# Optimization experiments

Measured on AMD Instinct MI355X. Metric: run time of the kernel, lower is better.

## Reference

```python
import jax, jax.numpy as jnp
import numpy as np

B, T, C = 4, 2048, 1024
H, D = 16, 64  # n_head, head_dim; H*D == C
EPS = 1e-12


def _l2norm(x):
    # matches torch F.normalize(dim=-1): x / max(||x||_2, eps)
    n = jnp.sqrt(jnp.sum(x * x, axis=-1, keepdims=True))
    return x / jnp.maximum(n, EPS)


def setup_inputs() -> dict:
    key = jax.random.key(0)
    ks = jax.random.split(key, 8)
    s = 0.02
    return {
        "x": jax.random.normal(ks[0], (B, T, C), dtype=jnp.float32),
        "Wq": jax.random.normal(ks[1], (C, C), dtype=jnp.float32) * s,
        "Wk": jax.random.normal(ks[2], (C, C), dtype=jnp.float32) * s,
        "Wv": jax.random.normal(ks[3], (C, C), dtype=jnp.float32) * s,
        "Wbeta": jax.random.normal(ks[4], (H, C), dtype=jnp.float32) * s,
        "bbeta": jnp.zeros((H,), dtype=jnp.float32),
        "Wgate": jax.random.normal(ks[5], (C, C), dtype=jnp.float32) * s,
        "Wo": jax.random.normal(ks[6], (C, C), dtype=jnp.float32) * s,
    }


def _forward(x, Wq, Wk, Wv, Wbeta, bbeta, Wgate, Wo):
    q = (x @ Wq.T).reshape(B, T, H, D)
    k = (x @ Wk.T).reshape(B, T, H, D)
    v = (x @ Wv.T).reshape(B, T, H, D)
    beta = jax.nn.sigmoid(x @ Wbeta.T + bbeta)  # (B,T,H)
    gate = jax.nn.sigmoid(x @ Wgate.T)          # (B,T,C)

    q = _l2norm(q)
    k = _l2norm(k)

    # time-major for scan: (T,B,H,D) / (T,B,H)
    qT = jnp.transpose(q, (1, 0, 2, 3))
    kT = jnp.transpose(k, (1, 0, 2, 3))
    vT = jnp.transpose(v, (1, 0, 2, 3))
    bT = jnp.transpose(beta, (1, 0, 2))

    M0 = jnp.zeros((B, H, D, D), dtype=x.dtype)

    def step(M, inp):
        q_t, k_t, v_t, b_t = inp
        o_t = jnp.einsum('bhdc,bhc->bhd', M, q_t)       # read state with q (pre-update)
        Mk = jnp.einsum('bhdc,bhc->bhd', M, k_t)
        dv = v_t - Mk                                    # delta-rule error
        M = M + b_t[..., None, None] * jnp.einsum('bhd,bhc->bhdc', dv, k_t)
        return M, o_t

    _, oT = jax.lax.scan(step, M0, (qT, kT, vT, bT))     # oT: (T,B,H,D)
    o = jnp.transpose(oT, (1, 0, 2, 3)).reshape(B, T, C)
    return (gate * o) @ Wo.T


def reference(x, Wq, Wk, Wv, Wbeta, bbeta, Wgate, Wo):
    return _forward(x, Wq, Wk, Wv, Wbeta, bbeta, Wgate, Wo)
```

## Files before the change

kernel.cpp:

```cpp
#include <hip/hip_runtime.h>
#include <cstdint>
#include <cstddef>

#define Bz 4
#define Tz 2048
#define Cz 1024
#define Hz 16
#define Dz 64
#define NTOK (Bz*Tz)
#define CHL 32
#define NCH (Tz/CHL)

typedef __attribute__((ext_vector_type(8))) short  short8;
typedef __attribute__((ext_vector_type(4))) float  floatx4;

__device__ __forceinline__ unsigned short f2bf(float x) {
  union { float f; uint32_t u; } a; a.f = x;
  uint32_t r = a.u + 0x7fffu + ((a.u >> 16) & 1u);
  return (unsigned short)(r >> 16);
}
__device__ __forceinline__ float bf2f(unsigned short u) {
  union { uint32_t i; float f; } a; a.i = ((uint32_t)u) << 16; return a.f;
}
__device__ __forceinline__ float sigmoidf_(float z) {
  return 1.0f / (1.0f + __expf(-z));
}
__device__ __forceinline__ uint32_t cvtpk_bf16(float a, float b) {
  uint32_t d;
  asm volatile("v_cvt_pk_bf16_f32 %0, %1, %2" : "=v"(d) : "v"(a), "v"(b));
  return d;
}
__device__ __forceinline__ float lo16f(uint32_t u) {
  union { uint32_t i; float f; } a; a.i = u << 16; return a.f;
}
__device__ __forceinline__ float hi16f(uint32_t u) {
  union { uint32_t i; float f; } a; a.i = u & 0xffff0000u; return a.f;
}

__device__ __forceinline__ void gload_lds16(const void* gptr, void* lptr) {
  __builtin_amdgcn_global_load_lds(
      (const __attribute__((address_space(1))) void*)(uintptr_t)gptr,
      (__attribute__((address_space(3))) void*)(uint32_t)(uintptr_t)lptr,
      16, 0, 0);
}

template<int CTRL>
__device__ __forceinline__ float dpp_addf(float x) {
  int y = __builtin_amdgcn_update_dpp(0, __float_as_int(x), CTRL, 0xF, 0xF, true);
  return x + __int_as_float(y);
}
__device__ __forceinline__ float rowsum16(float x) {
  x = dpp_addf<0xB1>(x);
  x = dpp_addf<0x4E>(x);
  x = dpp_addf<0x124>(x);
  x = dpp_addf<0x128>(x);
  return x;
}

union FragU { uint32_t u[4]; short8 s; };

__global__ __launch_bounds__(256) void cvt_bf16_kernel(const float* __restrict__ in,
                                                       unsigned short* __restrict__ out,
                                                       int n4) {
  int i = blockIdx.x * blockDim.x + threadIdx.x;
  int stride = gridDim.x * blockDim.x;
  const float4* in4 = (const float4*)in;
  ushort4* out4 = (ushort4*)out;
  for (; i < n4; i += stride) {
    float4 f = in4[i];
    ushort4 u;
    u.x = f2bf(f.x); u.y = f2bf(f.y); u.z = f2bf(f.z); u.w = f2bf(f.w);
    out4[i] = u;
  }
}

__global__ __launch_bounds__(256) void cvt_w5_kernel(
    const float* __restrict__ s0, const float* __restrict__ s1,
    const float* __restrict__ s2, const float* __restrict__ s3,
    const float* __restrict__ s4,
    unsigned short* __restrict__ d0, unsigned short* __restrict__ d1,
    unsigned short* __restrict__ d2, unsigned short* __restrict__ d3,
    unsigned short* __restrict__ d4, int n4)
{
  const int w = blockIdx.y;
  const float* s = (w == 0) ? s0 : (w == 1) ? s1 : (w == 2) ? s2 : (w == 3) ? s3 : s4;
  unsigned short* d = (w == 0) ? d0 : (w == 1) ? d1 : (w == 2) ? d2 : (w == 3) ? d3 : d4;
  int i = blockIdx.x * blockDim.x + threadIdx.x;
  if (i < n4) {
    float4 f = ((const float4*)s)[i];
    ushort4 u;
    u.x = f2bf(f.x); u.y = f2bf(f.y); u.z = f2bf(f.z); u.w = f2bf(f.w);
    ((ushort4*)d)[i] = u;
  }
}

#define VM8()  asm volatile("s_waitcnt vmcnt(8)" ::: "memory")
#define VM6()  asm volatile("s_waitcnt vmcnt(6)" ::: "memory")
#define VM4()  asm volatile("s_waitcnt vmcnt(4)" ::: "memory")
#define VM3()  asm volatile("s_waitcnt vmcnt(3)" ::: "memory")
#define VM0()  asm volatile("s_waitcnt vmcnt(0)" ::: "memory")
#define LGKM0() asm volatile("s_waitcnt lgkmcnt(0)" ::: "memory")
#define BARR() __builtin_amdgcn_s_barrier()

template<int BN, int OB16>
__global__ __launch_bounds__(512, 2) void gemm256_kernel(
    const unsigned short* __restrict__ A,
    const unsigned short* __restrict__ W0, const unsigned short* __restrict__ W1,
    const unsigned short* __restrict__ W2, const unsigned short* __restrict__ W3,
    void* __restrict__ O0, void* __restrict__ O1,
    void* __restrict__ O2, void* __restrict__ O3,
    int M, int N, int K, int nz_sigmoid, int norm_mask)
{
  constexpr int LB  = (BN == 256) ? 2 : 1;
  constexpr int NJ  = BN / 64;
  constexpr int AH  = 8192;
  constexpr int BH  = BN * 32;
  constexpr int PAR = 2 * AH + 2 * BH;
  __shared__ unsigned short smem[2 * PAR];

  const int gx = gridDim.x, gz = gridDim.z;
  const int nwg = gx * gridDim.y * gz;
  int flat = (blockIdx.z * gridDim.y + blockIdx.y) * gx + blockIdx.x;
  if ((nwg & 7) == 0) flat = (flat & 7) * (nwg >> 3) + (flat >> 3);
  const int xz = gx * gz;
  const int by = flat / xz;
  const int rem = flat - by * xz;
  const int bz = rem / gx;
  const int bx = rem - bz * gx;

  const unsigned short* Bw = (bz == 0) ? W0 : (bz == 1) ? W1 : (bz == 2) ? W2 : W3;
  void* Cw = (bz == 0) ? O0 : (bz == 1) ? O1 : (bz == 2) ? O2 : O3;
  const bool act = (bz == nz_sigmoid);
  const bool donorm = (norm_mask >> bz) & 1;

  const int m0 = by * 256, n0 = bx * BN;
  const int tid = threadIdx.x;
  const int wid = tid >> 6, lane = tid & 63;
  const int wm = wid >> 2, wn = wid & 3;
  const int ml = lane & 15, kq = lane >> 4;

  const unsigned short* Ap = A  + (size_t)m0 * K;
  const unsigned short* Bp = Bw + (size_t)n0 * K;

  const int srow = wid * 16 + (lane >> 2);
  const int ss8  = ((lane & 3) ^ ((lane >> 3) & 3)) * 8;
  const int rs8  = (kq ^ ((ml >> 1) & 3)) * 8;
  const int arow = wm * 128 + ml;
  const int brow = wn * (BN / 4) + ml;

  const int NT = K >> 6;
  const int hmax = NT << 2;

  floatx4 acc[8][NJ];
#pragma unroll
  for (int i = 0; i < 8; ++i)
#pragma unroll
    for (int j = 0; j < NJ; ++j) acc[i][j] = floatx4{0.f, 0.f, 0.f, 0.f};

#define HOFF(hh) ((hh) == 0 ? 0 : (hh) == 1 ? AH : (hh) == 2 ? AH + BH : 2 * AH + BH)
#define STAGE1(hsi) do {                                                      \
    const int ht_ = (hsi) >> 2, hh_ = (hsi) & 3;                              \
    const bool isB_ = hh_ & 1;                                                \
    const unsigned short* p_ = isB_ ? Bp : Ap;                                \
    const int kb_ = ht_ * 64 + (hh_ >> 1) * 32;                               \
    unsigned short* lb_ = &smem[(ht_ & 1) * PAR + HOFF(hh_) + wid * 512];     \
    gload_lds16(p_ + (size_t)srow * K + kb_ + ss8, lb_);                      \
    if (!isB_ || LB == 2)                                                     \
      gload_lds16(p_ + (size_t)(128 + srow) * K + kb_ + ss8, lb_ + 4096);     \
  } while (0)

  int hs = 0;
  for (; hs < 6 && hs < hmax; ++hs) STAGE1(hs);
  if constexpr (BN == 256) { VM8(); } else { VM6(); }
  BARR();

#define LOAD_A(Hb, mh)                                                        \
  _Pragma("unroll") for (int i = 0; i < 4; ++i)                               \
    af[i] = *(const short8*)&Hb[(arow + (mh) * 64 + i * 16) * 32 + rs8];
#define LOAD_B(Hb)                                                            \
  _Pragma("unroll") for (int j = 0; j < NJ; ++j)                              \
    bf[j] = *(const short8*)&Hb[(brow + j * 16) * 32 + rs8];
#define MFMA_Q(mh)                                                            \
  __builtin_amdgcn_s_setprio(1);                                              \
  _Pragma("unroll") for (int i = 0; i < 4; ++i)                               \
    _Pragma("unroll") for (int j = 0; j < NJ; ++j)                            \
      acc[(mh) * 4 + i][j] = __builtin_amdgcn_mfma_f32_16x16x32_bf16(         \
          af[i], bf[j], acc[(mh) * 4 + i][j], 0, 0, 0);                       \
  __builtin_amdgcn_s_setprio(0);
#define STAGE_NEXT() do { if (hs < hmax) { STAGE1(hs); ++hs; } } while (0)

  short8 af[4], bf[NJ];
  for (int t = 0; t < NT; ++t) {
    const unsigned short* Ah0 = &smem[(t & 1) * PAR + HOFF(0)];
    const unsigned short* Bh0 = &smem[(t & 1) * PAR + HOFF(1)];
    const unsigned short* Ah1 = &smem[(t & 1) * PAR + HOFF(2)];
    const unsigned short* Bh1 = &smem[(t & 1) * PAR + HOFF(3)];

    LOAD_A(Ah0, 0); LOAD_B(Bh0);
    STAGE_NEXT();
    BARR(); LGKM0();
    MFMA_Q(0);
    BARR();

    LOAD_A(Ah0, 1);
    STAGE_NEXT();
    BARR(); LGKM0();
    MFMA_Q(1);
    if (t == NT - 1) { VM0(); }
    else { if constexpr (BN == 256) { VM8(); } else { VM6(); } }
    BARR();

    LOAD_A(Ah1, 0); LOAD_B(Bh1);
    STAGE_NEXT();
    BARR(); LGKM0();
    MFMA_Q(0);
    BARR();

    LOAD_A(Ah1, 1);
    STAGE_NEXT();
    BARR(); LGKM0();
    MFMA_Q(1);
    if (t < NT - 2) { if constexpr (BN == 256) { VM8(); } else { VM6(); } }
    else if (t == NT - 2) { if constexpr (BN == 256) { VM4(); } else { VM3(); } }
    BARR();
  }

  float scale[8][4];
  if (donorm) {
#pragma unroll
    for (int i = 0; i < 8; ++i) {
#pragma unroll
      for (int r = 0; r < 4; ++r) {
        float ss = 0.f;
#pragma unroll
        for (int j = 0; j < NJ; ++j) ss = fmaf(acc[i][j][r], acc[i][j][r], ss);
        ss = rowsum16(ss);
        scale[i][r] = 1.0f / fmaxf(sqrtf(ss), 1e-12f);
      }
    }
  }

  const int row_base = m0 + wm * 128;
  const int col_base = n0 + wn * (BN / 4);
#pragma unroll
  for (int i = 0; i < 8; ++i) {
#pragma unroll
    for (int j = 0; j < NJ; ++j) {
      const int col = col_base + j * 16 + ml;
#pragma unroll
      for (int r = 0; r < 4; ++r) {
        const int row = row_base + i * 16 + kq * 4 + r;
        float val = acc[i][j][r];
        if (donorm) val *= scale[i][r];
        if (act) val = sigmoidf_(val);
        if constexpr (OB16) ((unsigned short*)Cw)[(size_t)row * N + col] = f2bf(val);
        else                ((float*)Cw)[(size_t)row * N + col] = val;
      }
    }
  }
}

__global__ __launch_bounds__(256) void beta_kernel(
    const float* __restrict__ x, const float* __restrict__ Wb,
    const float* __restrict__ bb, float* __restrict__ beta_out)
{
  const int n = blockIdx.x;
  const int wid = threadIdx.x >> 6;
  const int lane = threadIdx.x & 63;
  const float* xr = x + (size_t)n * Cz;
  for (int h = wid; h < Hz; h += 4) {
    const float* wr = Wb + (size_t)h * Cz;
    float s = 0.f;
#pragma unroll 4
    for (int i = lane; i < Cz; i += 64) s = fmaf(xr[i], wr[i], s);
#pragma unroll
    for (int ofs = 32; ofs >= 1; ofs >>= 1) s += __shfl_xor(s, ofs);
    if (lane == 0) beta_out[(size_t)n * Hz + h] = sigmoidf_(s + bb[h]);
  }
}

__global__ __launch_bounds__(256) void deltachunk_phase1(
    const unsigned short* __restrict__ qb, const unsigned short* __restrict__ kb,
    const unsigned short* __restrict__ vb, const float* __restrict__ betaf,
    float* __restrict__ of,
    unsigned short* __restrict__ qtb, unsigned short* __restrict__ wbuf,
    unsigned short* __restrict__ ubuf, unsigned short* __restrict__ ktb)
{
  __shared__ unsigned short Kb[32][72], Qb[32][72], Vb[32][72];
  __shared__ float As[32][36];
  __shared__ unsigned short Sb[32][40];
  __shared__ unsigned short Us[32][72], Ws[32][72], Qts[32][72];
  __shared__ float bsh[32];

  const int bid = blockIdx.x;
  const int chain = bid & 63;
  const int chunk = bid >> 6;
  const int b = chain >> 4, h = chain & 15;
  const int tid = threadIdx.x;
  const int wid = tid >> 6, lane = tid & 63;
  const int ml = lane & 15, kq = lane >> 4;

  const size_t tok0 = (size_t)b * Tz + (size_t)chunk * CHL;
  const size_t cb = ((size_t)chain * NCH + chunk) * 2048;

  {
    const int row = tid >> 3, c8 = (tid & 7) * 8;
    const size_t ga = (tok0 + row) * Cz + h * Dz + c8;
    *(uint4*)&Qb[row][c8] = *(const uint4*)&qb[ga];
    *(uint4*)&Kb[row][c8] = *(const uint4*)&kb[ga];
    *(uint4*)&Vb[row][c8] = *(const uint4*)&vb[ga];
  }
  if (tid < 32) bsh[tid] = betaf[(tok0 + tid) * Hz + h];
  __syncthreads();

  {
    const int tr = wid & 1, tc = wid >> 1;
    floatx4 accA = {0.f,0.f,0.f,0.f}, accS = {0.f,0.f,0.f,0.f};
#pragma unroll
    for (int eh = 0; eh < 2; ++eh) {
      short8 ka = *(const short8*)&Kb[tr * 16 + ml][eh * 32 + kq * 8];
      short8 kbf = *(const short8*)&Kb[tc * 16 + ml][eh * 32 + kq * 8];
      short8 qa = *(const short8*)&Qb[tr * 16 + ml][eh * 32 + kq * 8];
      accA = __builtin_amdgcn_mfma_f32_16x16x32_bf16(ka, kbf, accA, 0, 0, 0);
      accS = __builtin_amdgcn_mfma_f32_16x16x32_bf16(qa, kbf, accS, 0, 0, 0);
    }
#pragma unroll
    for (int r = 0; r < 4; ++r) {
      int t = tr * 16 + kq * 4 + r;
      int s = tc * 16 + ml;
      As[s][t] = bsh[t] * accA[r];
      Sb[t][s] = (t > s) ? f2bf(accS[r]) : (unsigned short)0;
    }
  }
  __syncthreads();

  if (tid < 128) {
    const int j = tid;
    float x[32];
    if (j < 64) {
#pragma unroll
      for (int t = 0; t < 32; ++t) x[t] = bsh[t] * bf2f(Vb[t][j]);
    } else {
#pragma unroll
      for (int t = 0; t < 32; ++t) x[t] = bsh[t] * bf2f(Kb[t][j - 64]);
    }
#pragma unroll
    for (int t = 0; t < 31; ++t) {
      float xt = x[t];
#pragma unroll
      for (int s = t + 1; s < 32; ++s) x[s] = fmaf(-As[t][s], xt, x[s]);
    }
    if (j < 64) {
#pragma unroll
      for (int t = 0; t < 32; ++t) Us[t][j] = f2bf(x[t]);
    } else {
#pragma unroll
      for (int t = 0; t < 32; ++t) Ws[t][j - 64] = f2bf(x[t]);
    }
  }
  __syncthreads();

  {
    const int dw = wid * 16 + ml;
    FragU bu, bw;
#pragma unroll
    for (int r = 0; r < 4; ++r) {
      bu.u[r] = (uint32_t)Us[kq * 8 + 2 * r][dw] | ((uint32_t)Us[kq * 8 + 2 * r + 1][dw] << 16);
      bw.u[r] = (uint32_t)Ws[kq * 8 + 2 * r][dw] | ((uint32_t)Ws[kq * 8 + 2 * r + 1][dw] << 16);
    }
    floatx4 accO[2], accQ[2];
#pragma unroll
    for (int tt = 0; tt < 2; ++tt) { accO[tt] = floatx4{0.f,0.f,0.f,0.f}; accQ[tt] = floatx4{0.f,0.f,0.f,0.f}; }
#pragma unroll
    for (int tt = 0; tt < 2; ++tt) {
      short8 sa = *(const short8*)&Sb[tt * 16 + ml][kq * 8];
      accO[tt] = __builtin_amdgcn_mfma_f32_16x16x32_bf16(sa, bu.s, accO[tt], 0, 0, 0);
      accQ[tt] = __builtin_amdgcn_mfma_f32_16x16x32_bf16(sa, bw.s, accQ[tt], 0, 0, 0);
    }
#pragma unroll
    for (int tt = 0; tt < 2; ++tt) {
#pragma unroll
      for (int r = 0; r < 4; ++r) {
        int t = tt * 16 + kq * 4 + r;
        of[(tok0 + t) * Cz + h * Dz + dw] = accO[tt][r];
        Qts[t][dw] = f2bf(bf2f(Qb[t][dw]) - accQ[tt][r]);
      }
    }
  }

  unsigned short ktmp[8], utmp[8];
  {
    const int e = tid >> 2, tq = (tid & 3) * 8;
#pragma unroll
    for (int i2 = 0; i2 < 8; ++i2) { ktmp[i2] = Kb[tq + i2][e]; utmp[i2] = Us[tq + i2][e]; }
  }
  __syncthreads();

  {
    const int row = tid >> 3, c8 = (tid & 7) * 8;
    const size_t o16 = cb + (size_t)row * 64 + c8;
    *(uint4*)&qtb[o16]  = *(const uint4*)&Qts[row][c8];
    *(uint4*)&wbuf[o16] = *(const uint4*)&Ws[row][c8];
    const int e = tid >> 2, tq = (tid & 3) * 8;
    *(uint4*)&ktb[cb + (size_t)e * 32 + tq]  = *(const uint4*)ktmp;
    *(uint4*)&ubuf[cb + (size_t)e * 32 + tq] = *(const uint4*)utmp;
  }
}

__global__ __launch_bounds__(256) void deltachunk_phase2(
    const unsigned short* __restrict__ qtb, const unsigned short* __restrict__ wbuf,
    const unsigned short* __restrict__ ubuf, const unsigned short* __restrict__ ktb,
    float* __restrict__ o2)
{
  __shared__ unsigned short Gb[2][64][72];
  __shared__ unsigned short Ub[2][32][40];
  __shared__ unsigned short Kts[2][64][40];
  __shared__ unsigned short Mh[2][32][72], Ml[2][32][72];

  const int chain = blockIdx.x >> 1;
  const int dh = blockIdx.x & 1;
  const int b = chain >> 4, h = chain & 15;
  const int d0 = dh * 32;
  const int tid = threadIdx.x;
  const int wid = tid >> 6, lane = tid & 63;
  const int ml = lane & 15, kq = lane >> 4;
  const int iq = wid >> 1, jq = wid & 1;

  const size_t cbase = (size_t)chain * NCH * 2048;

  const int grow = tid >> 2;
  const int gc16 = (tid & 3) * 16;
  const int ke   = tid >> 2;
  const int kc8  = (tid & 3) * 8;
  const int ue   = tid >> 3;
  const int uc4  = (tid & 7) * 4;

  const unsigned short* gsrc = (grow < 32) ? qtb : wbuf;
  const size_t gsoff = (size_t)(grow & 31) * 64 + gc16;

  {
    *(uint4*)&Gb[0][grow][gc16]     = *(const uint4*)&gsrc[cbase + gsoff];
    *(uint4*)&Gb[0][grow][gc16 + 8] = *(const uint4*)&gsrc[cbase + gsoff + 8];
    *(uint4*)&Kts[0][ke][kc8]       = *(const uint4*)&ktb[cbase + (size_t)ke * 32 + kc8];
    *(uint2*)&Ub[0][ue][uc4]        = *(const uint2*)&ubuf[cbase + (size_t)(d0 + ue) * 32 + uc4];
  }
  for (int i = tid; i < 32 * 72; i += 256) { (&Mh[0][0][0])[i] = 0; (&Ml[0][0][0])[i] = 0; }
  __syncthreads();

  const int idxA = (ml + 16 * ((kq & 1) * 2)) * 4;
  const int idxB = (ml + 16 * ((kq & 1) * 2 + 1)) * 4;
  const bool hiKq = (kq >= 2);

  floatx4 mAcc[4];
#pragma unroll
  for (int a = 0; a < 4; ++a) mAcc[a] = floatx4{0.f, 0.f, 0.f, 0.f};

  for (int c = 0; c < NCH; ++c) {
    const int cbuf = c & 1, nbuf = cbuf ^ 1;
    const int mr = c & 1, mw = mr ^ 1;
    const size_t tok0 = (size_t)b * Tz + (size_t)c * CHL;

    const int cn = (c + 1 < NCH) ? c + 1 : c;
    const size_t cbn = cbase + (size_t)cn * 2048;
    uint4 sg0 = *(const uint4*)&gsrc[cbn + gsoff];
    uint4 sg1 = *(const uint4*)&gsrc[cbn + gsoff + 8];
    uint4 sk  = *(const uint4*)&ktb[cbn + (size_t)ke * 32 + kc8];
    uint2 su  = *(const uint2*)&ubuf[cbn + (size_t)(d0 + ue) * 32 + uc4];

    floatx4 g1[2];
    g1[0] = floatx4{0.f,0.f,0.f,0.f}; g1[1] = floatx4{0.f,0.f,0.f,0.f};
#pragma unroll
    for (int eh = 0; eh < 2; ++eh) {
      short8 afr0 = *(const short8*)&Gb[cbuf][iq * 32 + 0  + ml][eh * 32 + kq * 8];
      short8 afr1 = *(const short8*)&Gb[cbuf][iq * 32 + 16 + ml][eh * 32 + kq * 8];
      short8 bh = *(const short8*)&Mh[mr][jq * 16 + ml][eh * 32 + kq * 8];
      short8 bl = *(const short8*)&Ml[mr][jq * 16 + ml][eh * 32 + kq * 8];
      g1[0] = __builtin_amdgcn_mfma_f32_16x16x32_bf16(afr0, bh, g1[0], 0, 0, 0);
      g1[0] = __builtin_amdgcn_mfma_f32_16x16x32_bf16(afr0, bl, g1[0], 0, 0, 0);
      g1[1] = __builtin_amdgcn_mfma_f32_16x16x32_bf16(afr1, bh, g1[1], 0, 0, 0);
      g1[1] = __builtin_amdgcn_mfma_f32_16x16x32_bf16(afr1, bl, g1[1], 0, 0, 0);
    }

    if (iq == 0) {
#pragma unroll
      for (int ti = 0; ti < 2; ++ti)
#pragma unroll
        for (int r = 0; r < 4; ++r)
          o2[(tok0 + ti * 16 + kq * 4 + r) * Cz + h * Dz + d0 + jq * 16 + ml] = g1[ti][r];
    } else {
      uint32_t pkh[2][2], pkl[2][2];
#pragma unroll
      for (int ti = 0; ti < 2; ++ti) {
        ushort4 uu = *(const ushort4*)&Ub[cbuf][jq * 16 + ml][ti * 16 + kq * 4];
        float z0 = bf2f(uu.x) - g1[ti][0];
        float z1 = bf2f(uu.y) - g1[ti][1];
        float z2 = bf2f(uu.z) - g1[ti][2];
        float z3 = bf2f(uu.w) - g1[ti][3];
        uint32_t h01 = cvtpk_bf16(z0, z1), h23 = cvtpk_bf16(z2, z3);
        pkh[ti][0] = h01; pkh[ti][1] = h23;
        pkl[ti][0] = cvtpk_bf16(z0 - lo16f(h01), z1 - hi16f(h01));
        pkl[ti][1] = cvtpk_bf16(z2 - lo16f(h23), z3 - hi16f(h23));
      }
      FragU zh, zl;
#pragma unroll
      for (int s = 0; s < 4; ++s) {
        const int idx = (s < 2) ? idxA : idxB;
        const int rp = s & 1;
        int v0 = __builtin_amdgcn_ds_bpermute(idx, (int)pkh[0][rp]);
        int v1 = __builtin_amdgcn_ds_bpermute(idx, (int)pkh[1][rp]);
        zh.u[s] = hiKq ? (uint32_t)v1 : (uint32_t)v0;
        int w0 = __builtin_amdgcn_ds_bpermute(idx, (int)pkl[0][rp]);
        int w1 = __builtin_amdgcn_ds_bpermute(idx, (int)pkl[1][rp]);
        zl.u[s] = hiKq ? (uint32_t)w1 : (uint32_t)w0;
      }
#pragma unroll
      for (int et = 0; et < 4; ++et) {
        short8 kfr = *(const short8*)&Kts[cbuf][et * 16 + ml][kq * 8];
        mAcc[et] = __builtin_amdgcn_mfma_f32_16x16x32_bf16(kfr, zh.s, mAcc[et], 0, 0, 0);
        mAcc[et] = __builtin_amdgcn_mfma_f32_16x16x32_bf16(kfr, zl.s, mAcc[et], 0, 0, 0);
      }
#pragma unroll
      for (int et = 0; et < 4; ++et) {
        float m0 = mAcc[et][0], m1 = mAcc[et][1], m2 = mAcc[et][2], m3 = mAcc[et][3];
        uint32_t h01 = cvtpk_bf16(m0, m1), h23 = cvtpk_bf16(m2, m3);
        uint32_t l01 = cvtpk_bf16(m0 - lo16f(h01), m1 - hi16f(h01));
        uint32_t l23 = cvtpk_bf16(m2 - lo16f(h23), m3 - hi16f(h23));
        *(uint2*)&Mh[mw][jq * 16 + ml][et * 16 + kq * 4] = make_uint2(h01, h23);
        *(uint2*)&Ml[mw][jq * 16 + ml][et * 16 + kq * 4] = make_uint2(l01, l23);
      }
    }

    *(uint4*)&Gb[nbuf][grow][gc16]     = sg0;
    *(uint4*)&Gb[nbuf][grow][gc16 + 8] = sg1;
    *(uint4*)&Kts[nbuf][ke][kc8]       = sk;
    *(uint2*)&Ub[nbuf][ue][uc4]        = su;

    LGKM0();
    BARR();
  }
}

__global__ __launch_bounds__(256) void gate_mul_kernel(
    const unsigned short* __restrict__ gsig, const float* __restrict__ o,
    const float* __restrict__ o2v, unsigned short* __restrict__ out, int n4)
{
  int i = blockIdx.x * blockDim.x + threadIdx.x;
  int stride = gridDim.x * blockDim.x;
  const ushort4* g4 = (const ushort4*)gsig;
  const float4* o4 = (const float4*)o;
  const float4* p4 = (const float4*)o2v;
  ushort4* out4 = (ushort4*)out;
  for (; i < n4; i += stride) {
    ushort4 gv = g4[i];
    float4 ov = o4[i];
    float4 pv = p4[i];
    ushort4 u;
    u.x = f2bf(bf2f(gv.x) * (ov.x + pv.x));
    u.y = f2bf(bf2f(gv.y) * (ov.y + pv.y));
    u.z = f2bf(bf2f(gv.z) * (ov.z + pv.z));
    u.w = f2bf(bf2f(gv.w) * (ov.w + pv.w));
    out4[i] = u;
  }
}

extern "C" void kernel_launch(void* const* d_in, const int* in_sizes, int n_in,
                              void* d_out, int out_size, void* d_ws, size_t ws_size,
                              hipStream_t stream) {
  const float* x     = (const float*)d_in[0];
  const float* Wq    = (const float*)d_in[1];
  const float* Wk    = (const float*)d_in[2];
  const float* Wv    = (const float*)d_in[3];
  const float* Wbeta = (const float*)d_in[4];
  const float* bbeta = (const float*)d_in[5];
  const float* Wgate = (const float*)d_in[6];
  const float* Wo    = (const float*)d_in[7];
  float* out = (float*)d_out;

  char* ws = (char*)d_ws;
  size_t off = 0;
  auto alloc = [&](size_t bytes) -> char* {
    char* p = ws + off;
    off += (bytes + 255) & ~(size_t)255;
    return p;
  };
  unsigned short* xb  = (unsigned short*)alloc((size_t)NTOK * Cz * 2);
  unsigned short* Wqb = (unsigned short*)alloc((size_t)Cz * Cz * 2);
  unsigned short* Wkb = (unsigned short*)alloc((size_t)Cz * Cz * 2);
  unsigned short* Wvb = (unsigned short*)alloc((size_t)Cz * Cz * 2);
  unsigned short* Wgb = (unsigned short*)alloc((size_t)Cz * Cz * 2);
  unsigned short* Wob = (unsigned short*)alloc((size_t)Cz * Cz * 2);
  unsigned short* qb  = (unsigned short*)alloc((size_t)NTOK * Cz * 2);
  unsigned short* kb  = (unsigned short*)alloc((size_t)NTOK * Cz * 2);
  unsigned short* vb  = (unsigned short*)alloc((size_t)NTOK * Cz * 2);
  unsigned short* gb  = (unsigned short*)alloc((size_t)NTOK * Cz * 2);
  float* of    = (float*)alloc((size_t)NTOK * Cz * 4);
  float* o2    = (float*)alloc((size_t)NTOK * Cz * 4);
  float* betaf = (float*)alloc((size_t)NTOK * Hz * 4);
  unsigned short* qtb  = (unsigned short*)alloc((size_t)64 * NCH * 2048 * 2);
  unsigned short* wbuf = (unsigned short*)alloc((size_t)64 * NCH * 2048 * 2);
  unsigned short* ubuf = (unsigned short*)alloc((size_t)64 * NCH * 2048 * 2);
  unsigned short* ktb  = (unsigned short*)alloc((size_t)64 * NCH * 2048 * 2);
  unsigned short* ab = xb;

  const int n4x = NTOK * Cz / 4;
  const int n4w = Cz * Cz / 4;

  cvt_bf16_kernel<<<dim3(1024), dim3(256), 0, stream>>>(x, xb, n4x);
  cvt_w5_kernel<<<dim3(n4w / 256, 5), dim3(256), 0, stream>>>(
      Wq, Wk, Wv, Wgate, Wo, Wqb, Wkb, Wvb, Wgb, Wob, n4w);

  gemm256_kernel<256, 1><<<dim3(Cz / 256, NTOK / 256, 4), dim3(512), 0, stream>>>(
      xb, Wqb, Wkb, Wvb, Wgb, qb, kb, vb, gb, NTOK, Cz, Cz, 3, 3);

  beta_kernel<<<dim3(NTOK), dim3(256), 0, stream>>>(x, Wbeta, bbeta, betaf);

  deltachunk_phase1<<<dim3(64 * NCH), dim3(256), 0, stream>>>(
      qb, kb, vb, betaf, of, qtb, wbuf, ubuf, ktb);
  deltachunk_phase2<<<dim3(128), dim3(256), 0, stream>>>(qtb, wbuf, ubuf, ktb, o2);

  gate_mul_kernel<<<dim3(1024), dim3(256), 0, stream>>>(gb, of, o2, ab, n4x);

  gemm256_kernel<128, 0><<<dim3(Cz / 128, NTOK / 256, 1), dim3(512), 0, stream>>>(
      ab, Wob, Wob, Wob, Wob, out, out, out, out, NTOK, Cz, Cz, -1, 0);
}
```

Before: 370.7 us.

## Fuse gate multiply into delta-rule phase2 and merge conversion kernels

```diff
diff --git a/kernel.cpp b/kernel.cpp
--- a/kernel.cpp
+++ b/kernel.cpp
@@ -59,38 +59,28 @@
 
 union FragU { uint32_t u[4]; short8 s; };
 
-__global__ __launch_bounds__(256) void cvt_bf16_kernel(const float* __restrict__ in,
-                                                       unsigned short* __restrict__ out,
-                                                       int n4) {
+__global__ __launch_bounds__(256) void cvt6_kernel(
+    const float* __restrict__ s0, const float* __restrict__ s1,
+    const float* __restrict__ s2, const float* __restrict__ s3,
+    const float* __restrict__ s4, const float* __restrict__ s5,
+    unsigned short* __restrict__ d0, unsigned short* __restrict__ d1,
+    unsigned short* __restrict__ d2, unsigned short* __restrict__ d3,
+    unsigned short* __restrict__ d4, unsigned short* __restrict__ d5,
+    int n4x, int n4w)
+{
+  const int w = blockIdx.y;
+  const float* s = (w == 0) ? s0 : (w == 1) ? s1 : (w == 2) ? s2 : (w == 3) ? s3 : (w == 4) ? s4 : s5;
+  unsigned short* d = (w == 0) ? d0 : (w == 1) ? d1 : (w == 2) ? d2 : (w == 3) ? d3 : (w == 4) ? d4 : d5;
+  const int n4 = (w == 0) ? n4x : n4w;
   int i = blockIdx.x * blockDim.x + threadIdx.x;
   int stride = gridDim.x * blockDim.x;
-  const float4* in4 = (const float4*)in;
-  ushort4* out4 = (ushort4*)out;
+  const float4* in4 = (const float4*)s;
+  ushort4* out4 = (ushort4*)d;
   for (; i < n4; i += stride) {
     float4 f = in4[i];
     ushort4 u;
     u.x = f2bf(f.x); u.y = f2bf(f.y); u.z = f2bf(f.z); u.w = f2bf(f.w);
     out4[i] = u;
-  }
-}
-
-__global__ __launch_bounds__(256) void cvt_w5_kernel(
-    const float* __restrict__ s0, const float* __restrict__ s1,
-    const float* __restrict__ s2, const float* __restrict__ s3,
-    const float* __restrict__ s4,
-    unsigned short* __restrict__ d0, unsigned short* __restrict__ d1,
-    unsigned short* __restrict__ d2, unsigned short* __restrict__ d3,
-    unsigned short* __restrict__ d4, int n4)
-{
-  const int w = blockIdx.y;
-  const float* s = (w == 0) ? s0 : (w == 1) ? s1 : (w == 2) ? s2 : (w == 3) ? s3 : s4;
-  unsigned short* d = (w == 0) ? d0 : (w == 1) ? d1 : (w == 2) ? d2 : (w == 3) ? d3 : d4;
-  int i = blockIdx.x * blockDim.x + threadIdx.x;
-  if (i < n4) {
-    float4 f = ((const float4*)s)[i];
-    ushort4 u;
-    u.x = f2bf(f.x); u.y = f2bf(f.y); u.z = f2bf(f.z); u.w = f2bf(f.w);
-    ((ushort4*)d)[i] = u;
   }
 }
 
@@ -410,7 +400,8 @@
 __global__ __launch_bounds__(256) void deltachunk_phase2(
     const unsigned short* __restrict__ qtb, const unsigned short* __restrict__ wbuf,
     const unsigned short* __restrict__ ubuf, const unsigned short* __restrict__ ktb,
-    float* __restrict__ o2)
+    const unsigned short* __restrict__ gbuf, const float* __restrict__ ofv,
+    unsigned short* __restrict__ ab)
 {
   __shared__ unsigned short Gb[2][64][72];
   __shared__ unsigned short Ub[2][32][40];
@@ -427,6 +418,7 @@
   const int iq = wid >> 1, jq = wid & 1;
 
   const size_t cbase = (size_t)chain * NCH * 2048;
+  const int gcol = h * Dz + d0 + jq * 16 + ml;
 
   const int grow = tid >> 2;
   const int gc16 = (tid & 3) * 16;
@@ -438,11 +430,23 @@
   const unsigned short* gsrc = (grow < 32) ? qtb : wbuf;
   const size_t gsoff = (size_t)(grow & 31) * 64 + gc16;
 
+  unsigned short pg[8]; float pf[8];
   {
     *(uint4*)&Gb[0][grow][gc16]     = *(const uint4*)&gsrc[cbase + gsoff];
     *(uint4*)&Gb[0][grow][gc16 + 8] = *(const uint4*)&gsrc[cbase + gsoff + 8];
     *(uint4*)&Kts[0][ke][kc8]       = *(const uint4*)&ktb[cbase + (size_t)ke * 32 + kc8];
     *(uint2*)&Ub[0][ue][uc4]        = *(const uint2*)&ubuf[cbase + (size_t)(d0 + ue) * 32 + uc4];
+  }
+  if (iq == 0) {
+    const size_t t0 = (size_t)b * Tz;
+#pragma unroll
+    for (int ti = 0; ti < 2; ++ti)
+#pragma unroll
+      for (int r = 0; r < 4; ++r) {
+        const size_t gi = (t0 + ti * 16 + kq * 4 + r) * Cz + gcol;
+        pg[ti * 4 + r] = gbuf[gi];
+        pf[ti * 4 + r] = ofv[gi];
+      }
   }
   for (int i = tid; i < 32 * 72; i += 256) { (&Mh[0][0][0])[i] = 0; (&Ml[0][0][0])[i] = 0; }
   __syncthreads();
@@ -466,6 +470,18 @@
     uint4 sg1 = *(const uint4*)&gsrc[cbn + gsoff + 8];
     uint4 sk  = *(const uint4*)&ktb[cbn + (size_t)ke * 32 + kc8];
     uint2 su  = *(const uint2*)&ubuf[cbn + (size_t)(d0 + ue) * 32 + uc4];
+    unsigned short ng[8]; float nf[8];
+    if (iq == 0) {
+      const size_t tkn = (size_t)b * Tz + (size_t)cn * CHL;
+#pragma unroll
+      for (int ti = 0; ti < 2; ++ti)
+#pragma unroll
+        for (int r = 0; r < 4; ++r) {
+          const size_t gi = (tkn + ti * 16 + kq * 4 + r) * Cz + gcol;
+          ng[ti * 4 + r] = gbuf[gi];
+          nf[ti * 4 + r] = ofv[gi];
+        }
+    }
 
     floatx4 g1[2];
     g1[0] = floatx4{0.f,0.f,0.f,0.f}; g1[1] = floatx4{0.f,0.f,0.f,0.f};
@@ -485,8 +501,13 @@
 #pragma unroll
       for (int ti = 0; ti < 2; ++ti)
 #pragma unroll
-        for (int r = 0; r < 4; ++r)
-          o2[(tok0 + ti * 16 + kq * 4 + r) * Cz + h * Dz + d0 + jq * 16 + ml] = g1[ti][r];
+        for (int r = 0; r < 4; ++r) {
+          const size_t gi = (tok0 + ti * 16 + kq * 4 + r) * Cz + gcol;
+          const float val = bf2f(pg[ti * 4 + r]) * (pf[ti * 4 + r] + g1[ti][r]);
+          ab[gi] = f2bf(val);
+        }
+#pragma unroll
+      for (int e = 0; e < 8; ++e) { pg[e] = ng[e]; pf[e] = nf[e]; }
     } else {
       uint32_t pkh[2][2], pkl[2][2];
 #pragma unroll
@@ -537,29 +558,6 @@
 
     LGKM0();
     BARR();
-  }
-}
-
-__global__ __launch_bounds__(256) void gate_mul_kernel(
-    const unsigned short* __restrict__ gsig, const float* __restrict__ o,
-    const float* __restrict__ o2v, unsigned short* __restrict__ out, int n4)
-{
-  int i = blockIdx.x * blockDim.x + threadIdx.x;
-  int stride = gridDim.x * blockDim.x;
-  const ushort4* g4 = (const ushort4*)gsig;
-  const float4* o4 = (const float4*)o;
-  const float4* p4 = (const float4*)o2v;
-  ushort4* out4 = (ushort4*)out;
-  for (; i < n4; i += stride) {
-    ushort4 gv = g4[i];
-    float4 ov = o4[i];
-    float4 pv = p4[i];
-    ushort4 u;
-    u.x = f2bf(bf2f(gv.x) * (ov.x + pv.x));
-    u.y = f2bf(bf2f(gv.y) * (ov.y + pv.y));
-    u.z = f2bf(bf2f(gv.z) * (ov.z + pv.z));
-    u.w = f2bf(bf2f(gv.w) * (ov.w + pv.w));
-    out4[i] = u;
   }
 }
 
@@ -594,7 +592,6 @@
   unsigned short* vb  = (unsigned short*)alloc((size_t)NTOK * Cz * 2);
   unsigned short* gb  = (unsigned short*)alloc((size_t)NTOK * Cz * 2);
   float* of    = (float*)alloc((size_t)NTOK * Cz * 4);
-  float* o2    = (float*)alloc((size_t)NTOK * Cz * 4);
   float* betaf = (float*)alloc((size_t)NTOK * Hz * 4);
   unsigned short* qtb  = (unsigned short*)alloc((size_t)64 * NCH * 2048 * 2);
   unsigned short* wbuf = (unsigned short*)alloc((size_t)64 * NCH * 2048 * 2);
@@ -605,9 +602,8 @@
   const int n4x = NTOK * Cz / 4;
   const int n4w = Cz * Cz / 4;
 
-  cvt_bf16_kernel<<<dim3(1024), dim3(256), 0, stream>>>(x, xb, n4x);
-  cvt_w5_kernel<<<dim3(n4w / 256, 5), dim3(256), 0, stream>>>(
-      Wq, Wk, Wv, Wgate, Wo, Wqb, Wkb, Wvb, Wgb, Wob, n4w);
+  cvt6_kernel<<<dim3(1024, 6), dim3(256), 0, stream>>>(
+      x, Wq, Wk, Wv, Wgate, Wo, xb, Wqb, Wkb, Wvb, Wgb, Wob, n4x, n4w);
 
   gemm256_kernel<256, 1><<<dim3(Cz / 256, NTOK / 256, 4), dim3(512), 0, stream>>>(
       xb, Wqb, Wkb, Wvb, Wgb, qb, kb, vb, gb, NTOK, Cz, Cz, 3, 3);
@@ -616,9 +612,9 @@
 
   deltachunk_phase1<<<dim3(64 * NCH), dim3(256), 0, stream>>>(
       qb, kb, vb, betaf, of, qtb, wbuf, ubuf, ktb);
-  deltachunk_phase2<<<dim3(128), dim3(256), 0, stream>>>(qtb, wbuf, ubuf, ktb, o2);
-
-  gate_mul_kernel<<<dim3(1024), dim3(256), 0, stream>>>(gb, of, o2, ab, n4x);
+
+  deltachunk_phase2<<<dim3(128), dim3(256), 0, stream>>>(
+      qtb, wbuf, ubuf, ktb, gb, of, ab);
 
   gemm256_kernel<128, 0><<<dim3(Cz / 128, NTOK / 256, 1), dim3(512), 0, stream>>>(
       ab, Wob, Wob, Wob, Wob, out, out, out, out, NTOK, Cz, Cz, -1, 0);
```

New measurement: 366.9 us (median of 4 runs). Within noise of the previous version (-1.0%).
